# Kernel optimization log

Hardware: AMD Instinct MI355X
Metric: run time of the kernel (lower is better)

Reference implementation:

```python
import jax, jax.numpy as jnp
import numpy as np

B, A, G = 2, 256, 65536  # batch, num_atoms (= sum(Z)), num_grid_points


def setup_inputs() -> dict:
    key = jax.random.key(0)
    k1, k2, k3 = jax.random.split(key, 3)
    R_tensor = jax.random.normal(k1, (B, A, 3), dtype=jnp.float32)
    coords = jax.random.normal(k2, (G, 3), dtype=jnp.float32)
    weight = jax.random.normal(k3, (3, 3), dtype=jnp.float32)  # 'exp_matrix' param
    Z = jnp.ones((A,), dtype=jnp.int32)  # atomic numbers; sum(Z) == A
    return {"R_tensor": R_tensor, "coords": coords, "weight": weight, "Z": Z}


def reference(R_tensor, coords, weight, Z):
    # diff[b, g, a, :] = coords[g] - R_tensor[b, a]   -> (B, G, A, 3)
    diff = coords[None, :, None, :] - R_tensor[:, None, :, :]
    # tf.einsum('ijkl,ml->ijkm', diff, weight): apply 3x3 transform on last axis
    t = jnp.einsum('bgal,ml->bgam', diff, weight)
    # Euclidean norm over last axis -> (B, G, A)
    d = jnp.sqrt(jnp.sum(t * t, axis=-1))
    # exp then reduce over atoms -> (B, G)
    return jnp.sum(jnp.exp(d), axis=2)
```

## Files before the change

kernel.cpp:

```cpp
#include <hip/hip_runtime.h>
#include <math.h>

#define NB 2
#define NA 256
#define NG 65536

__global__ __launch_bounds__(256) void init_layer_kernel(
    const float* __restrict__ R,
    const float* __restrict__ coords,
    const float* __restrict__ W,
    float* __restrict__ out)
{
    __shared__ float4 sWr[NA];

    const int b   = blockIdx.y;
    const int tid = threadIdx.x;

    const float w00 = W[0], w01 = W[1], w02 = W[2];
    const float w10 = W[3], w11 = W[4], w12 = W[5];
    const float w20 = W[6], w21 = W[7], w22 = W[8];

    {
        const int base = (b * NA + tid) * 3;
        const float rx = R[base + 0];
        const float ry = R[base + 1];
        const float rz = R[base + 2];
        sWr[tid] = make_float4(w00 * rx + w01 * ry + w02 * rz,
                               w10 * rx + w11 * ry + w12 * rz,
                               w20 * rx + w21 * ry + w22 * rz,
                               0.0f);
    }
    __syncthreads();

    const int g  = blockIdx.x * blockDim.x + tid;
    const float cx = coords[g * 3 + 0];
    const float cy = coords[g * 3 + 1];
    const float cz = coords[g * 3 + 2];

    const float tx = w00 * cx + w01 * cy + w02 * cz;
    const float ty = w10 * cx + w11 * cy + w12 * cz;
    const float tz = w20 * cx + w21 * cy + w22 * cz;

    float s0 = 0.0f, s1 = 0.0f, s2 = 0.0f, s3 = 0.0f;

    #pragma unroll 8
    for (int a = 0; a < NA; a += 4) {
        const float4 r0 = sWr[a + 0];
        const float4 r1 = sWr[a + 1];
        const float4 r2 = sWr[a + 2];
        const float4 r3 = sWr[a + 3];

        {
            const float dx = tx - r0.x, dy = ty - r0.y, dz = tz - r0.z;
            s0 += __expf(sqrtf(dx * dx + dy * dy + dz * dz));
        }
        {
            const float dx = tx - r1.x, dy = ty - r1.y, dz = tz - r1.z;
            s1 += __expf(sqrtf(dx * dx + dy * dy + dz * dz));
        }
        {
            const float dx = tx - r2.x, dy = ty - r2.y, dz = tz - r2.z;
            s2 += __expf(sqrtf(dx * dx + dy * dy + dz * dz));
        }
        {
            const float dx = tx - r3.x, dy = ty - r3.y, dz = tz - r3.z;
            s3 += __expf(sqrtf(dx * dx + dy * dy + dz * dz));
        }
    }

    out[b * NG + g] = (s0 + s1) + (s2 + s3);
}

extern "C" void kernel_launch(void* const* d_in, const int* in_sizes, int n_in,
                              void* d_out, int out_size, void* d_ws, size_t ws_size,
                              hipStream_t stream) {
    const float* R      = (const float*)d_in[0];
    const float* coords = (const float*)d_in[1];
    const float* W      = (const float*)d_in[2];
    float* out = (float*)d_out;

    dim3 grid(NG / 256, NB);
    dim3 block(256);
    init_layer_kernel<<<grid, block, 0, stream>>>(R, coords, W, out);
}
```

Before: 83.35 us.

## Expand squared distance algebraically, use native exp2/sqrt, split atoms across waves

Atom positions are transformed once by a separate precompute kernel into workspace, pre-scaled by log2(e), so each distance becomes |t|^2 - 2t·r + |r|^2 evaluated with three FMAs and fed to native exp2 and sqrt builtins. Each block now covers 64 grid points, with its four waves each handling a quarter of the atoms read via scalar/uniform loads, and the partial sums are combined through shared memory. This removes the per-block LDS staging and cuts ALU work per pair. In exchange it adds a second launch, risks cancellation error in the expanded distance (clamped at zero), and uses builtins that may be less accurate than the previous calls.

```diff
diff --git a/kernel.cpp b/kernel.cpp
--- a/kernel.cpp
+++ b/kernel.cpp
@@ -5,70 +5,94 @@
 #define NA 256
 #define NG 65536
 
+#define LOG2E 1.4426950408889634074f
+
+#if __has_builtin(__builtin_amdgcn_sqrtf)
+#define FSQRT(x) __builtin_amdgcn_sqrtf(x)
+#else
+#define FSQRT(x) sqrtf(x)
+#endif
+
+#if __has_builtin(__builtin_amdgcn_exp2f)
+#define FEXP2(x) __builtin_amdgcn_exp2f(x)
+#else
+#define FEXP2(x) __expf((x) * 0.69314718055994530942f)
+#endif
+
+__global__ __launch_bounds__(512) void precompute_atoms(
+    const float* __restrict__ R,
+    const float* __restrict__ W,
+    float4* __restrict__ ws)
+{
+    const int i = threadIdx.x;
+    const float w00 = W[0], w01 = W[1], w02 = W[2];
+    const float w10 = W[3], w11 = W[4], w12 = W[5];
+    const float w20 = W[6], w21 = W[7], w22 = W[8];
+    const float rx = R[i * 3 + 0];
+    const float ry = R[i * 3 + 1];
+    const float rz = R[i * 3 + 2];
+    const float sx = LOG2E * (w00 * rx + w01 * ry + w02 * rz);
+    const float sy = LOG2E * (w10 * rx + w11 * ry + w12 * rz);
+    const float sz = LOG2E * (w20 * rx + w21 * ry + w22 * rz);
+    ws[i] = make_float4(-2.0f * sx, -2.0f * sy, -2.0f * sz,
+                        sx * sx + sy * sy + sz * sz);
+}
+
 __global__ __launch_bounds__(256) void init_layer_kernel(
-    const float* __restrict__ R,
     const float* __restrict__ coords,
     const float* __restrict__ W,
+    const float4* __restrict__ ws,
     float* __restrict__ out)
 {
-    __shared__ float4 sWr[NA];
-
-    const int b   = blockIdx.y;
-    const int tid = threadIdx.x;
+    const int tid   = threadIdx.x;
+    const int gl    = tid & 63;
+    const int slice = __builtin_amdgcn_readfirstlane(tid >> 6);
+    const int b     = blockIdx.y;
+    const int g     = blockIdx.x * 64 + gl;
 
     const float w00 = W[0], w01 = W[1], w02 = W[2];
     const float w10 = W[3], w11 = W[4], w12 = W[5];
     const float w20 = W[6], w21 = W[7], w22 = W[8];
 
-    {
-        const int base = (b * NA + tid) * 3;
-        const float rx = R[base + 0];
-        const float ry = R[base + 1];
-        const float rz = R[base + 2];
-        sWr[tid] = make_float4(w00 * rx + w01 * ry + w02 * rz,
-                               w10 * rx + w11 * ry + w12 * rz,
-                               w20 * rx + w21 * ry + w22 * rz,
-                               0.0f);
-    }
-    __syncthreads();
-
-    const int g  = blockIdx.x * blockDim.x + tid;
     const float cx = coords[g * 3 + 0];
     const float cy = coords[g * 3 + 1];
     const float cz = coords[g * 3 + 2];
 
-    const float tx = w00 * cx + w01 * cy + w02 * cz;
-    const float ty = w10 * cx + w11 * cy + w12 * cz;
-    const float tz = w20 * cx + w21 * cy + w22 * cz;
+    const float tx = LOG2E * (w00 * cx + w01 * cy + w02 * cz);
+    const float ty = LOG2E * (w10 * cx + w11 * cy + w12 * cz);
+    const float tz = LOG2E * (w20 * cx + w21 * cy + w22 * cz);
+    const float t2 = tx * tx + ty * ty + tz * tz;
+
+    const float4* __restrict__ wsb = ws + b * NA + slice * 64;
 
     float s0 = 0.0f, s1 = 0.0f, s2 = 0.0f, s3 = 0.0f;
 
-    #pragma unroll 8
-    for (int a = 0; a < NA; a += 4) {
-        const float4 r0 = sWr[a + 0];
-        const float4 r1 = sWr[a + 1];
-        const float4 r2 = sWr[a + 2];
-        const float4 r3 = sWr[a + 3];
+    #pragma unroll 4
+    for (int a = 0; a < 64; a += 4) {
+        const float4 p0 = wsb[a + 0];
+        const float4 p1 = wsb[a + 1];
+        const float4 p2 = wsb[a + 2];
+        const float4 p3 = wsb[a + 3];
 
-        {
-            const float dx = tx - r0.x, dy = ty - r0.y, dz = tz - r0.z;
-            s0 += __expf(sqrtf(dx * dx + dy * dy + dz * dz));
-        }
-        {
-            const float dx = tx - r1.x, dy = ty - r1.y, dz = tz - r1.z;
-            s1 += __expf(sqrtf(dx * dx + dy * dy + dz * dz));
-        }
-        {
-            const float dx = tx - r2.x, dy = ty - r2.y, dz = tz - r2.z;
-            s2 += __expf(sqrtf(dx * dx + dy * dy + dz * dz));
-        }
-        {
-            const float dx = tx - r3.x, dy = ty - r3.y, dz = tz - r3.z;
-            s3 += __expf(sqrtf(dx * dx + dy * dy + dz * dz));
-        }
+        const float d0 = fmaf(p0.x, tx, fmaf(p0.y, ty, fmaf(p0.z, tz, p0.w + t2)));
+        const float d1 = fmaf(p1.x, tx, fmaf(p1.y, ty, fmaf(p1.z, tz, p1.w + t2)));
+        const float d2 = fmaf(p2.x, tx, fmaf(p2.y, ty, fmaf(p2.z, tz, p2.w + t2)));
+        const float d3 = fmaf(p3.x, tx, fmaf(p3.y, ty, fmaf(p3.z, tz, p3.w + t2)));
+
+        s0 += FEXP2(FSQRT(fmaxf(d0, 0.0f)));
+        s1 += FEXP2(FSQRT(fmaxf(d1, 0.0f)));
+        s2 += FEXP2(FSQRT(fmaxf(d2, 0.0f)));
+        s3 += FEXP2(FSQRT(fmaxf(d3, 0.0f)));
     }
 
-    out[b * NG + g] = (s0 + s1) + (s2 + s3);
+    __shared__ float red[256];
+    red[tid] = (s0 + s1) + (s2 + s3);
+    __syncthreads();
+
+    if (tid < 64) {
+        out[b * NG + blockIdx.x * 64 + tid] =
+            (red[tid] + red[tid + 64]) + (red[tid + 128] + red[tid + 192]);
+    }
 }
 
 extern "C" void kernel_launch(void* const* d_in, const int* in_sizes, int n_in,
@@ -77,9 +101,11 @@
     const float* R      = (const float*)d_in[0];
     const float* coords = (const float*)d_in[1];
     const float* W      = (const float*)d_in[2];
-    float* out = (float*)d_out;
+    float* out  = (float*)d_out;
+    float4* ws4 = (float4*)d_ws;
 
-    dim3 grid(NG / 256, NB);
-    dim3 block(256);
-    init_layer_kernel<<<grid, block, 0, stream>>>(R, coords, W, out);
+    precompute_atoms<<<dim3(1), dim3(NB * NA), 0, stream>>>(R, W, ws4);
+
+    dim3 grid(NG / 64, NB);
+    init_layer_kernel<<<grid, dim3(256), 0, stream>>>(coords, W, ws4, out);
 }
```

Measured after the change: 68.94 us. -17.3%, faster.
